# Optimization experiments

Measured on AMD Instinct MI355X. Metric: run time of the kernel, lower is better.

## Reference

```python
import jax, jax.numpy as jnp
import numpy as np

S = 4096
V = 50000
E = 512
H = 512
CE = 128
CH = 128
T = 50


def _lstm_dir(x, W_ih, W_hh, b, reverse):
    # x: [S, D]; PyTorch gate order i, f, g, o. b = b_ih + b_hh fused.
    gx = x @ W_ih.T + b  # [S, 4H] precomputed input contribution
    Hd = W_hh.shape[1]
    def step(carry, g_t):
        h, c = carry
        g = g_t + h @ W_hh.T
        i, f, gg, o = jnp.split(g, 4, axis=-1)
        c = jax.nn.sigmoid(f) * c + jax.nn.sigmoid(i) * jnp.tanh(gg)
        h = jax.nn.sigmoid(o) * jnp.tanh(c)
        return (h, c), h
    init = (jnp.zeros((Hd,), x.dtype), jnp.zeros((Hd,), x.dtype))
    _, hs = jax.lax.scan(step, init, gx, reverse=reverse)
    return hs  # [S, H]


def _bilstm(x, Wih_f, Whh_f, b_f, Wih_b, Whh_b, b_b):
    fwd = _lstm_dir(x, Wih_f, Whh_f, b_f, False)
    bwd = _lstm_dir(x, Wih_b, Whh_b, b_b, True)
    return jnp.concatenate([fwd, bwd], axis=-1)  # [S, 2H]


def _viterbi(emissions, start_t, end_t, trans):
    # emissions: [S, T]. Standard CRF Viterbi (torchcrf semantics).
    score0 = start_t + emissions[0]  # [T]
    def step(score, emit):
        m = score[:, None] + trans          # [T_prev, T_cur]
        bp = jnp.argmax(m, axis=0)          # best previous tag for each cur tag
        new_score = jnp.max(m, axis=0) + emit
        return new_score, bp
    final, bps = jax.lax.scan(step, score0, emissions[1:])  # bps: [S-1, T]
    final = final + end_t
    last = jnp.argmax(final)
    def back(tag, bp):
        prev = bp[tag]
        return prev, prev
    _, path_head = jax.lax.scan(back, last, bps, reverse=True)  # [S-1]
    return jnp.concatenate([path_head, last[None]])  # [S]


def setup_inputs() -> dict:
    key = jax.random.key(0)
    ks = jax.random.split(key, 20)
    s = 0.05
    inp = {
        'sentence': jax.random.randint(ks[0], (S,), 0, V),
        'char_sentence': jax.random.randint(ks[1], (S,), 0, V),
        'word_emb': jax.random.normal(ks[2], (V, E), jnp.float32) * s,
        'char_emb': jax.random.normal(ks[3], (V, CE), jnp.float32) * s,
        # char BiLSTM
        'cWih_f': jax.random.normal(ks[4], (4 * CH, CE), jnp.float32) * s,
        'cWhh_f': jax.random.normal(ks[5], (4 * CH, CH), jnp.float32) * s,
        'cb_f': jnp.zeros((4 * CH,), jnp.float32),
        'cWih_b': jax.random.normal(ks[6], (4 * CH, CE), jnp.float32) * s,
        'cWhh_b': jax.random.normal(ks[7], (4 * CH, CH), jnp.float32) * s,
        'cb_b': jnp.zeros((4 * CH,), jnp.float32),
        # word BiLSTM (input dim E + 2*CH)
        'wWih_f': jax.random.normal(ks[8], (4 * H, E + 2 * CH), jnp.float32) * s,
        'wWhh_f': jax.random.normal(ks[9], (4 * H, H), jnp.float32) * s,
        'wb_f': jnp.zeros((4 * H,), jnp.float32),
        'wWih_b': jax.random.normal(ks[10], (4 * H, E + 2 * CH), jnp.float32) * s,
        'wWhh_b': jax.random.normal(ks[11], (4 * H, H), jnp.float32) * s,
        'wb_b': jnp.zeros((4 * H,), jnp.float32),
        # hidden2tag
        'W_tag': jax.random.normal(ks[12], (T, 2 * H), jnp.float32) * s,
        'b_tag': jnp.zeros((T,), jnp.float32),
        # CRF params
        'start_t': jax.random.normal(ks[13], (T,), jnp.float32) * s,
        'end_t': jax.random.normal(ks[14], (T,), jnp.float32) * s,
        'trans': jax.random.normal(ks[15], (T, T), jnp.float32) * s,
    }
    return inp


def reference(sentence, char_sentence, word_emb, char_emb,
              cWih_f, cWhh_f, cb_f, cWih_b, cWhh_b, cb_b,
              wWih_f, wWhh_f, wb_f, wWih_b, wWhh_b, wb_b,
              W_tag, b_tag, start_t, end_t, trans):
    we = word_emb[sentence]          # [S, E]
    ce = char_emb[char_sentence]     # [S, CE]
    char_out = _bilstm(ce, cWih_f, cWhh_f, cb_f, cWih_b, cWhh_b, cb_b)  # [S, 2*CH]
    emb = jnp.concatenate([we, char_out], axis=-1)  # [S, E + 2*CH]
    lstm_out = _bilstm(emb, wWih_f, wWhh_f, wb_f, wWih_b, wWhh_b, wb_b)  # [S, 2H]
    tag_space = lstm_out @ W_tag.T + b_tag  # [S, T] emissions
    path = _viterbi(tag_space, start_t, end_t, trans)  # [S] int32 tags
    return path
```

## Files before the change

kernel.cpp:

```cpp
#include <hip/hip_runtime.h>
#include <math.h>

#define SQ   4096
#define EDIM 512
#define CEDIM 128
#define CHH  128
#define WH   512
#define NT   50

typedef unsigned long long ull;

__device__ __forceinline__ float sigf(float x) { return 1.0f / (1.0f + expf(-x)); }

#define PIN4(V) asm volatile("" : "+v"(V.x), "+v"(V.y), "+v"(V.z), "+v"(V.w));

__device__ __forceinline__ void ld8x_sc0(const ull* p, ull& q0, ull& q1, ull& q2,
                                         ull& q3, ull& q4, ull& q5, ull& q6, ull& q7) {
    asm volatile("global_load_dwordx2 %0, %8, off sc0\n\t"
                 "global_load_dwordx2 %1, %8, off offset:8 sc0\n\t"
                 "global_load_dwordx2 %2, %8, off offset:16 sc0\n\t"
                 "global_load_dwordx2 %3, %8, off offset:24 sc0\n\t"
                 "global_load_dwordx2 %4, %8, off offset:32 sc0\n\t"
                 "global_load_dwordx2 %5, %8, off offset:40 sc0\n\t"
                 "global_load_dwordx2 %6, %8, off offset:48 sc0\n\t"
                 "global_load_dwordx2 %7, %8, off offset:56 sc0\n\t"
                 "s_waitcnt vmcnt(0)"
                 : "=&v"(q0), "=&v"(q1), "=&v"(q2), "=&v"(q3),
                   "=&v"(q4), "=&v"(q5), "=&v"(q6), "=&v"(q7)
                 : "v"(p) : "memory");
}
__device__ __forceinline__ ull ld_mir(const ull* p) {
    return __hip_atomic_load(p, __ATOMIC_RELAXED, __HIP_MEMORY_SCOPE_AGENT);
}
__device__ __forceinline__ void st_plain8(ull* p, ull v) {
    asm volatile("global_store_dwordx2 %0, %1, off" :: "v"(p), "v"(v) : "memory");
}
__device__ __forceinline__ void st_mir(ull* p, ull v) {
    __hip_atomic_store(p, v, __ATOMIC_RELAXED, __HIP_MEMORY_SCOPE_AGENT);
}
__device__ __forceinline__ unsigned umin2(unsigned a, unsigned b) { return a < b ? a : b; }

#define FMA4(W, off) { float4 h4 = *(const float4*)&hc[off]; \
    a0 += W.x * h4.x; a1 += W.y * h4.y; a2 += W.z * h4.z; a3 += W.w * h4.w; }

__global__ __launch_bounds__(256) void k1_gather_cgx(
    const int* __restrict__ sent, const int* __restrict__ csent,
    const float* __restrict__ wemb, const float* __restrict__ cemb,
    const float* __restrict__ cWih_f, const float* __restrict__ cb_f,
    const float* __restrict__ cWih_b, const float* __restrict__ cb_b,
    float* __restrict__ we_g, float* __restrict__ cgx)
{
    const int tid = threadIdx.x;
    const int t0 = blockIdx.x * 16;
    __shared__ __align__(16) float ceL[16][128];
    __shared__ int sids[16], cids[16];
    if (tid < 16) sids[tid] = sent[t0 + tid];
    else if (tid < 32) cids[tid - 16] = csent[t0 + tid - 16];
    __syncthreads();
    {
        int f4 = tid;
        for (int q = 0; q < 2; ++q, f4 += 256) {
            int r = f4 >> 5, k4 = f4 & 31;
            float4 v = *(const float4*)&cemb[(size_t)cids[r] * CEDIM + k4 * 4];
            *(float4*)&ceL[r][k4 * 4] = v;
        }
    }
    {
        int f4 = tid;
        for (int q = 0; q < 8; ++q, f4 += 256) {
            int r = f4 >> 7, k4 = f4 & 127;
            float4 v = *(const float4*)&wemb[(size_t)sids[r] * EDIM + k4 * 4];
            *(float4*)&we_g[(size_t)(t0 + r) * EDIM + k4 * 4] = v;
        }
    }
    __syncthreads();
    for (int q = 0; q < 4; ++q) {
        int j = q * 256 + tid;
        int d = j >> 9, r = j & 511;
        const float* Wih = d ? cWih_b : cWih_f;
        const float* cb = d ? cb_b : cb_f;
        float b = cb[r];
        float acc[16];
#pragma unroll
        for (int tt = 0; tt < 16; ++tt) acc[tt] = b;
        for (int k4 = 0; k4 < 32; ++k4) {
            float4 wv = *(const float4*)&Wih[r * CEDIM + k4 * 4];
#pragma unroll
            for (int tt = 0; tt < 16; ++tt) {
                acc[tt] += wv.x * ceL[tt][k4 * 4 + 0] + wv.y * ceL[tt][k4 * 4 + 1]
                         + wv.z * ceL[tt][k4 * 4 + 2] + wv.w * ceL[tt][k4 * 4 + 3];
            }
        }
#pragma unroll
        for (int tt = 0; tt < 16; ++tt)
            cgx[((size_t)d * SQ + (t0 + tt)) * 512 + r] = acc[tt];
    }
}

__global__ __launch_bounds__(1024, 4) void k2_charlstm_gemm(
    const float* __restrict__ cWhh_f, const float* __restrict__ cWhh_b,
    const float* __restrict__ cgx, float* __restrict__ cho,
    const float* __restrict__ we_g,
    const float* __restrict__ wWih_f, const float* __restrict__ wb_f,
    const float* __restrict__ wWih_b, const float* __restrict__ wb_b,
    float* __restrict__ wgx)
{
    const int tid = threadIdx.x;
    __shared__ __align__(16) float At[32][68];
    __shared__ __align__(16) float Bt[32][128];
    __shared__ __align__(16) float hstC[128];
    __shared__ float partC[2][516];
    __shared__ float trC[512];

    if (blockIdx.x < 2) {
        const int dir = blockIdx.x;
        const float* Whh = dir ? cWhh_b : cWhh_f;
        const int row = tid & 511;
        const int half = tid >> 9;
        const float4* wp = (const float4*)&Whh[(size_t)row * CHH + half * 64];
        float4 w0 = wp[0], w1 = wp[1], w2 = wp[2], w3 = wp[3];
        float4 w4 = wp[4], w5 = wp[5], w6 = wp[6], w7 = wp[7];
        float4 w8 = wp[8], w9 = wp[9], w10 = wp[10], w11 = wp[11];
        float4 w12 = wp[12], w13 = wp[13], w14 = wp[14], w15 = wp[15];
        PIN4(w0) PIN4(w1) PIN4(w2) PIN4(w3) PIN4(w4) PIN4(w5) PIN4(w6) PIN4(w7)
        PIN4(w8) PIN4(w9) PIN4(w10) PIN4(w11) PIN4(w12) PIN4(w13) PIN4(w14) PIN4(w15)

        const float* gxc = cgx + (size_t)dir * SQ * 512;
        float cst = 0.f;
        if (tid < 32) *(float4*)&hstC[tid * 4] = make_float4(0, 0, 0, 0);
        __syncthreads();
        for (int t = 0; t < SQ; ++t) {
            const int x = dir ? (SQ - 1 - t) : t;
            float gxv = (tid < 512) ? gxc[(size_t)x * 512 + tid] : 0.f;
            float a0 = 0.f, a1 = 0.f, a2 = 0.f, a3 = 0.f;
            const float* hc = &hstC[half * 64];
            FMA4(w0, 0)   FMA4(w1, 4)   FMA4(w2, 8)   FMA4(w3, 12)
            FMA4(w4, 16)  FMA4(w5, 20)  FMA4(w6, 24)  FMA4(w7, 28)
            FMA4(w8, 32)  FMA4(w9, 36)  FMA4(w10, 40) FMA4(w11, 44)
            FMA4(w12, 48) FMA4(w13, 52) FMA4(w14, 56) FMA4(w15, 60)
            partC[half][row] = (a0 + a1) + (a2 + a3);
            __syncthreads();
            if (tid < 512) {
                float s = partC[0][tid] + partC[1][tid] + gxv;
                const bool isg = ((tid >> 7) == 2);
                float y = sigf(isg ? (s + s) : s);
                trC[tid] = isg ? (y + y - 1.f) : y;
            }
            __syncthreads();
            if (tid < 128) {
                float iv = trC[tid], fv = trC[128 + tid];
                float gv = trC[256 + tid], ov = trC[384 + tid];
                cst = fv * cst + iv * gv;
                float ts = sigf(cst + cst);
                float h = ov * (ts + ts - 1.f);
                hstC[tid] = h;
                cho[(size_t)x * 256 + dir * CHH + tid] = h;
            }
            __syncthreads();
        }
        return;
    }
    const int tile = blockIdx.x - 2;
    const int dir = tile >> 10;
    const int rem = tile & 1023;
    const int mb = rem >> 4;
    const int nb = rem & 15;
    const float* Wih = dir ? wWih_b : wWih_f;
    const float* wb = dir ? wb_b : wb_f;
    float* C = wgx + (size_t)dir * SQ * 2048;
    const int tm = tid >> 6, tn = tid & 63;
    float acc[4][2];
#pragma unroll
    for (int i = 0; i < 4; ++i) { acc[i][0] = 0.f; acc[i][1] = 0.f; }
    for (int kb = 0; kb < 16; ++kb) {
        if (tid < 512) {
            int rowm = tid >> 3, k4 = tid & 7;
            float4 v = *(const float4*)&we_g[(size_t)(mb * 64 + rowm) * EDIM + kb * 32 + k4 * 4];
            At[k4 * 4 + 0][rowm] = v.x; At[k4 * 4 + 1][rowm] = v.y;
            At[k4 * 4 + 2][rowm] = v.z; At[k4 * 4 + 3][rowm] = v.w;
        }
        {
            int rr = tid >> 3, k4 = tid & 7;
            float4 v = *(const float4*)&Wih[(size_t)(nb * 128 + rr) * 768 + kb * 32 + k4 * 4];
            Bt[k4 * 4 + 0][rr] = v.x; Bt[k4 * 4 + 1][rr] = v.y;
            Bt[k4 * 4 + 2][rr] = v.z; Bt[k4 * 4 + 3][rr] = v.w;
        }
        __syncthreads();
#pragma unroll
        for (int kk = 0; kk < 32; ++kk) {
            float4 a4 = *(const float4*)&At[kk][tm * 4];
            float2 b2 = *(const float2*)&Bt[kk][tn * 2];
            acc[0][0] += a4.x * b2.x; acc[0][1] += a4.x * b2.y;
            acc[1][0] += a4.y * b2.x; acc[1][1] += a4.y * b2.y;
            acc[2][0] += a4.z * b2.x; acc[2][1] += a4.z * b2.y;
            acc[3][0] += a4.w * b2.x; acc[3][1] += a4.w * b2.y;
        }
        __syncthreads();
    }
    float2 wbv = *(const float2*)&wb[nb * 128 + tn * 2];
#pragma unroll
    for (int i = 0; i < 4; ++i) {
        float2 o;
        o.x = acc[i][0] + wbv.x; o.y = acc[i][1] + wbv.y;
        *(float2*)&C[(size_t)(mb * 64 + tm * 4 + i) * 2048 + nb * 128 + tn * 2] = o;
    }
}

__global__ __launch_bounds__(512, 2) void k3_gemm_char(
    const float* __restrict__ cho,
    const float* __restrict__ wWih_f, const float* __restrict__ wWih_b,
    float* __restrict__ wgx)
{
    const int tid = threadIdx.x;
    const int tile = blockIdx.x;
    const int dir = tile >> 10;
    const int rem = tile & 1023;
    const int mb = rem >> 4, nb = rem & 15;
    const float* Wih = dir ? wWih_b : wWih_f;
    float* C = wgx + (size_t)dir * SQ * 2048;
    __shared__ __align__(16) float At[32][68];
    __shared__ __align__(16) float Bt[32][128];
    const int tm = tid >> 5, tn = tid & 31;
    float acc[4][4];
#pragma unroll
    for (int i = 0; i < 4; ++i)
#pragma unroll
        for (int jj = 0; jj < 4; ++jj) acc[i][jj] = 0.f;
    for (int kb = 0; kb < 8; ++kb) {
        {
            int rowm = tid >> 3, k4 = tid & 7;
            float4 v = *(const float4*)&cho[(size_t)(mb * 64 + rowm) * 256 + kb * 32 + k4 * 4];
            At[k4 * 4 + 0][rowm] = v.x; At[k4 * 4 + 1][rowm] = v.y;
            At[k4 * 4 + 2][rowm] = v.z; At[k4 * 4 + 3][rowm] = v.w;
        }
#pragma unroll
        for (int q = 0; q < 2; ++q) {
            int f4 = q * 512 + tid;
            int rr = f4 >> 3, k4 = f4 & 7;
            float4 v = *(const float4*)&Wih[(size_t)(nb * 128 + rr) * 768 + 512 + kb * 32 + k4 * 4];
            Bt[k4 * 4 + 0][rr] = v.x; Bt[k4 * 4 + 1][rr] = v.y;
            Bt[k4 * 4 + 2][rr] = v.z; Bt[k4 * 4 + 3][rr] = v.w;
        }
        __syncthreads();
#pragma unroll
        for (int kk = 0; kk < 32; ++kk) {
            float4 a4 = *(const float4*)&At[kk][tm * 4];
            float4 b4 = *(const float4*)&Bt[kk][tn * 4];
            acc[0][0] += a4.x * b4.x; acc[0][1] += a4.x * b4.y; acc[0][2] += a4.x * b4.z; acc[0][3] += a4.x * b4.w;
            acc[1][0] += a4.y * b4.x; acc[1][1] += a4.y * b4.y; acc[1][2] += a4.y * b4.z; acc[1][3] += a4.y * b4.w;
            acc[2][0] += a4.z * b4.x; acc[2][1] += a4.z * b4.y; acc[2][2] += a4.z * b4.z; acc[2][3] += a4.z * b4.w;
            acc[3][0] += a4.w * b4.x; acc[3][1] += a4.w * b4.y; acc[3][2] += a4.w * b4.z; acc[3][3] += a4.w * b4.w;
        }
        __syncthreads();
    }
#pragma unroll
    for (int i = 0; i < 4; ++i) {
        float* cp = &C[(size_t)(mb * 64 + tm * 4 + i) * 2048 + nb * 128 + tn * 4];
        float4 o = *(float4*)cp;
        o.x += acc[i][0]; o.y += acc[i][1]; o.z += acc[i][2]; o.w += acc[i][3];
        *(float4*)cp = o;
    }
}

__global__ __launch_bounds__(1024, 4) void k4_word_lstm(
    const float* __restrict__ wWhh_f, const float* __restrict__ wWhh_b,
    const float* __restrict__ wgx, float* __restrict__ lstm, ull* __restrict__ pairs)
{
    const int res = blockIdx.x & 7;
    if (res > 1) return;
    const int dir = res;
    const int wid = blockIdx.x >> 3;
    const int tid = threadIdx.x;
    const int k = tid >> 6;
    const int r = tid & 63;
    const int g = r >> 4, u = r & 15;
    const float* Whh = dir ? wWhh_b : wWhh_f;
    const int G = g * WH + wid * 16 + u;
    const float4* wp = (const float4*)&Whh[(size_t)G * WH + k * 32];
    float4 w0 = wp[0], w1 = wp[1], w2 = wp[2], w3 = wp[3];
    float4 w4 = wp[4], w5 = wp[5], w6 = wp[6], w7 = wp[7];
    PIN4(w0) PIN4(w1) PIN4(w2) PIN4(w3) PIN4(w4) PIN4(w5) PIN4(w6) PIN4(w7)

    __shared__ __align__(16) float hst[512];
    __shared__ float part[16][65];

    ull* wpf = pairs;
    ull* wpm = pairs + 2048;
    const float* gx = wgx + (size_t)dir * SQ * 2048;
    float cst = 0.f;
    int useFast = 1, alive = 1;
    for (int t = 0; t < SQ; ++t) {
        const int x = dir ? (SQ - 1 - t) : t;
        float gxv = 0.f;
        if (tid < 64)
            gxv = gx[(size_t)x * 2048 + (size_t)(tid >> 4) * 512 + wid * 16 + (tid & 15)];
        if (t == 0) {
            if (tid < 128) *(float4*)&hst[tid * 4] = make_float4(0, 0, 0, 0);
        } else if (tid < 64) {
            const size_t boff = ((size_t)((t - 1) & 1) * 2 + dir) * 512 + tid * 8;
            const ull* pf = wpf + boff;
            const ull* pm = wpm + boff;
            ull q0 = 0, q1 = 0, q2 = 0, q3 = 0, q4 = 0, q5 = 0, q6 = 0, q7 = 0;
            int spins = 0;
            while (alive) {
                if (useFast) {
                    ld8x_sc0(pf, q0, q1, q2, q3, q4, q5, q6, q7);
                } else {
                    q0 = ld_mir(pm + 0); q1 = ld_mir(pm + 1);
                    q2 = ld_mir(pm + 2); q3 = ld_mir(pm + 3);
                    q4 = ld_mir(pm + 4); q5 = ld_mir(pm + 5);
                    q6 = ld_mir(pm + 6); q7 = ld_mir(pm + 7);
                }
                unsigned tm = umin2(umin2(umin2((unsigned)(q0 >> 32), (unsigned)(q1 >> 32)),
                                          umin2((unsigned)(q2 >> 32), (unsigned)(q3 >> 32))),
                                    umin2(umin2((unsigned)(q4 >> 32), (unsigned)(q5 >> 32)),
                                          umin2((unsigned)(q6 >> 32), (unsigned)(q7 >> 32))));
                if (__all(tm >= (unsigned)t)) break;
                ++spins;
                if (useFast && spins > 2048) { useFast = 0; spins = 0; }
                if (!useFast && spins > (1 << 20)) alive = 0;
                __builtin_amdgcn_s_sleep(1);
            }
            float* hd = &hst[tid * 8];
            hd[0] = __uint_as_float((unsigned)q0); hd[1] = __uint_as_float((unsigned)q1);
            hd[2] = __uint_as_float((unsigned)q2); hd[3] = __uint_as_float((unsigned)q3);
            hd[4] = __uint_as_float((unsigned)q4); hd[5] = __uint_as_float((unsigned)q5);
            hd[6] = __uint_as_float((unsigned)q6); hd[7] = __uint_as_float((unsigned)q7);
        }
        __syncthreads();
        float a0 = 0.f, a1 = 0.f, a2 = 0.f, a3 = 0.f;
        const float* hc = &hst[k * 32];
        FMA4(w0, 0)  FMA4(w1, 4)  FMA4(w2, 8)  FMA4(w3, 12)
        FMA4(w4, 16) FMA4(w5, 20) FMA4(w6, 24) FMA4(w7, 28)
        part[k][r] = (a0 + a1) + (a2 + a3);
        __syncthreads();
        if (tid < 64) {
            float s = gxv;
#pragma unroll
            for (int kk = 0; kk < 16; ++kk) s += part[kk][tid];
            const bool isg = ((tid >> 4) == 2);
            float y = sigf(isg ? (s + s) : s);
            float val = isg ? (y + y - 1.f) : y;
            float fv = __shfl(val, 16 + (tid & 15));
            float gv = __shfl(val, 32 + (tid & 15));
            float ov = __shfl(val, 48 + (tid & 15));
            if (tid < 16) {
                cst = fv * cst + val * gv;
                float ts = sigf(cst + cst);
                float h = ov * (ts + ts - 1.f);
                const int unit = wid * 16 + tid;
                lstm[(size_t)x * 1024 + dir * WH + unit] = h;
                ull q = ((ull)(unsigned)(t + 1) << 32) | (ull)__float_as_uint(h);
                const size_t poff = ((size_t)(t & 1) * 2 + dir) * 512 + unit;
                st_plain8(wpf + poff, q);
                st_mir(wpm + poff, q);
            }
        }
    }
}

__global__ __launch_bounds__(64) void k5_emis(
    const float* __restrict__ lstm, const float* __restrict__ Wtag,
    const float* __restrict__ btag, float* __restrict__ emis)
{
    const int t = blockIdx.x, tid = threadIdx.x;
    __shared__ __align__(16) float rowL[1024];
#pragma unroll
    for (int q = 0; q < 4; ++q) {
        int f4 = q * 64 + tid;
        *(float4*)&rowL[f4 * 4] = *(const float4*)&lstm[(size_t)t * 1024 + f4 * 4];
    }
    __syncthreads();
    if (tid < NT) {
        float a0 = 0.f, a1 = 0.f, a2 = 0.f, a3 = 0.f;
        const float* wr = Wtag + (size_t)tid * 1024;
        for (int k4 = 0; k4 < 256; ++k4) {
            float4 wv = *(const float4*)&wr[k4 * 4];
            a0 += wv.x * rowL[k4 * 4 + 0];
            a1 += wv.y * rowL[k4 * 4 + 1];
            a2 += wv.z * rowL[k4 * 4 + 2];
            a3 += wv.w * rowL[k4 * 4 + 3];
        }
        emis[(size_t)t * NT + tid] = btag[tid] + (a0 + a1) + (a2 + a3);
    }
}

__global__ __launch_bounds__(256) void k6a_viterbi(
    const float* __restrict__ emis, const float* __restrict__ start_t,
    const float* __restrict__ end_t, const float* __restrict__ trans,
    unsigned char* __restrict__ bpb, int* __restrict__ last)
{
    const int tid = threadIdx.x;
    const int g = tid >> 6, c = tid & 63;
    __shared__ float sc[64];
    __shared__ float pbest[4][64];
    __shared__ int pbp[4][64];
    const int p0 = g * 13;
    float tr[13];
#pragma unroll
    for (int i = 0; i < 13; ++i) {
        int p = p0 + i;
        tr[i] = (c < NT && p < NT) ? trans[p * NT + c] : -1e30f;
    }
    if (tid < 64) sc[tid] = (tid < NT) ? (start_t[tid] + emis[tid]) : -1e30f;
    __syncthreads();
    for (int t = 1; t < SQ; ++t) {
        float best = -1e30f; int bp = 0;
#pragma unroll
        for (int i = 0; i < 13; ++i) {
            float v = sc[p0 + i] + tr[i];
            if (v > best) { best = v; bp = p0 + i; }
        }
        pbest[g][c] = best; pbp[g][c] = bp;
        __syncthreads();
        if (tid < NT) {
            float b = pbest[0][tid]; int bb = pbp[0][tid];
#pragma unroll
            for (int gg = 1; gg < 4; ++gg) {
                float v = pbest[gg][tid];
                if (v > b) { b = v; bb = pbp[gg][tid]; }
            }
            bpb[(size_t)t * NT + tid] = (unsigned char)bb;
            sc[tid] = b + emis[(size_t)t * NT + tid];
        }
        __syncthreads();
    }
    if (tid == 0) {
        float b = -1e30f; int bi = 0;
        for (int cc = 0; cc < NT; ++cc) {
            float v = sc[cc] + end_t[cc];
            if (v > b) { b = v; bi = cc; }
        }
        *last = bi;
    }
}

__global__ __launch_bounds__(64) void k6b_maps(
    const unsigned char* __restrict__ bpb, int* __restrict__ map_)
{
    const int k = blockIdx.x;
    const int e = threadIdx.x;
    if (k == 0 || e >= NT) return;
    int tag = e;
    for (int i = 63; i >= 0; --i) {
        int t = k * 64 + i;
        tag = bpb[(size_t)t * NT + tag];
    }
    map_[k * NT + e] = tag;
}

__global__ __launch_bounds__(64) void k6c_backtrack(
    const unsigned char* __restrict__ bpb, const int* __restrict__ map_,
    const int* __restrict__ last, int* __restrict__ path)
{
    __shared__ int B[64];
    if (threadIdx.x == 0) {
        int tag = *last;
        B[63] = tag;
        for (int k = 63; k >= 1; --k) {
            tag = map_[k * NT + tag];
            B[k - 1] = tag;
        }
    }
    __syncthreads();
    const int k = threadIdx.x;
    int tag = B[k];
    for (int i = 63; i >= 0; --i) {
        int t = k * 64 + i;
        path[t] = tag;
        if (t >= 1) tag = bpb[(size_t)t * NT + tag];
    }
}

extern "C" void kernel_launch(void* const* d_in, const int* in_sizes, int n_in,
                              void* d_out, int out_size, void* d_ws, size_t ws_size,
                              hipStream_t stream)
{
    const int* sent = (const int*)d_in[0];
    const int* csent = (const int*)d_in[1];
    const float* wemb = (const float*)d_in[2];
    const float* cemb = (const float*)d_in[3];
    const float* cWih_f = (const float*)d_in[4];
    const float* cWhh_f = (const float*)d_in[5];
    const float* cb_f = (const float*)d_in[6];
    const float* cWih_b = (const float*)d_in[7];
    const float* cWhh_b = (const float*)d_in[8];
    const float* cb_b = (const float*)d_in[9];
    const float* wWih_f = (const float*)d_in[10];
    const float* wWhh_f = (const float*)d_in[11];
    const float* wb_f = (const float*)d_in[12];
    const float* wWih_b = (const float*)d_in[13];
    const float* wWhh_b = (const float*)d_in[14];
    const float* wb_b = (const float*)d_in[15];
    const float* Wtag = (const float*)d_in[16];
    const float* btag = (const float*)d_in[17];
    const float* start_t = (const float*)d_in[18];
    const float* end_t = (const float*)d_in[19];
    const float* trans = (const float*)d_in[20];
    int* path = (int*)d_out;

    float* ws = (float*)d_ws;
    float* we_g = ws;
    float* cgx  = we_g + (size_t)SQ * EDIM;
    float* cho  = cgx + (size_t)2 * SQ * 512;
    float* wgx  = cho + (size_t)SQ * 256;
    float* lstm = wgx + (size_t)2 * SQ * 2048;
    float* emis = lstm + (size_t)SQ * 1024;
    ull* pairs  = (ull*)(emis + (size_t)SQ * NT);
    int* map_   = (int*)(pairs + 5120);
    int* lastp  = map_ + 64 * NT;
    unsigned char* bpb = (unsigned char*)(lastp + 4);

    (void)hipMemsetAsync(pairs, 0, 5120 * sizeof(ull), stream);

    k1_gather_cgx<<<SQ / 16, 256, 0, stream>>>(sent, csent, wemb, cemb,
                                               cWih_f, cb_f, cWih_b, cb_b, we_g, cgx);
    k2_charlstm_gemm<<<2 + 2048, 1024, 0, stream>>>(cWhh_f, cWhh_b, cgx, cho, we_g,
                                                    wWih_f, wb_f, wWih_b, wb_b, wgx);
    k3_gemm_char<<<2048, 512, 0, stream>>>(cho, wWih_f, wWih_b, wgx);
    k4_word_lstm<<<256, 1024, 0, stream>>>(wWhh_f, wWhh_b, wgx, lstm, pairs);
    k5_emis<<<SQ, 64, 0, stream>>>(lstm, Wtag, btag, emis);
    k6a_viterbi<<<1, 256, 0, stream>>>(emis, start_t, end_t, trans, bpb, lastp);
    k6b_maps<<<64, 64, 0, stream>>>(bpb, map_);
    k6c_backtrack<<<1, 64, 0, stream>>>(bpb, map_, lastp, path);
}
```

Measured before the change: 14.14 ms.

## Let each wave poll its own h slice and drop a barrier in LSTM loops

```diff
diff --git a/kernel.cpp b/kernel.cpp
--- a/kernel.cpp
+++ b/kernel.cpp
@@ -14,20 +14,9 @@
 
 #define PIN4(V) asm volatile("" : "+v"(V.x), "+v"(V.y), "+v"(V.z), "+v"(V.w));
 
-__device__ __forceinline__ void ld8x_sc0(const ull* p, ull& q0, ull& q1, ull& q2,
-                                         ull& q3, ull& q4, ull& q5, ull& q6, ull& q7) {
-    asm volatile("global_load_dwordx2 %0, %8, off sc0\n\t"
-                 "global_load_dwordx2 %1, %8, off offset:8 sc0\n\t"
-                 "global_load_dwordx2 %2, %8, off offset:16 sc0\n\t"
-                 "global_load_dwordx2 %3, %8, off offset:24 sc0\n\t"
-                 "global_load_dwordx2 %4, %8, off offset:32 sc0\n\t"
-                 "global_load_dwordx2 %5, %8, off offset:40 sc0\n\t"
-                 "global_load_dwordx2 %6, %8, off offset:48 sc0\n\t"
-                 "global_load_dwordx2 %7, %8, off offset:56 sc0\n\t"
-                 "s_waitcnt vmcnt(0)"
-                 : "=&v"(q0), "=&v"(q1), "=&v"(q2), "=&v"(q3),
-                   "=&v"(q4), "=&v"(q5), "=&v"(q6), "=&v"(q7)
-                 : "v"(p) : "memory");
+__device__ __forceinline__ ull ld1_sc0(const ull* p) {
+    ull q; asm volatile("global_load_dwordx2 %0, %1, off sc0\n\ts_waitcnt vmcnt(0)"
+                        : "=v"(q) : "v"(p) : "memory"); return q;
 }
 __device__ __forceinline__ ull ld_mir(const ull* p) {
     return __hip_atomic_load(p, __ATOMIC_RELAXED, __HIP_MEMORY_SCOPE_AGENT);
@@ -38,7 +27,6 @@
 __device__ __forceinline__ void st_mir(ull* p, ull v) {
     __hip_atomic_store(p, v, __ATOMIC_RELAXED, __HIP_MEMORY_SCOPE_AGENT);
 }
-__device__ __forceinline__ unsigned umin2(unsigned a, unsigned b) { return a < b ? a : b; }
 
 #define FMA4(W, off) { float4 h4 = *(const float4*)&hc[off]; \
     a0 += W.x * h4.x; a1 += W.y * h4.y; a2 += W.z * h4.z; a3 += W.w * h4.w; }
@@ -110,7 +98,6 @@
     __shared__ __align__(16) float Bt[32][128];
     __shared__ __align__(16) float hstC[128];
     __shared__ float partC[2][516];
-    __shared__ float trC[512];
 
     if (blockIdx.x < 2) {
         const int dir = blockIdx.x;
@@ -127,29 +114,38 @@
 
         const float* gxc = cgx + (size_t)dir * SQ * 512;
         float cst = 0.f;
+        float gxp0 = 0.f, gxp1 = 0.f;
+        if (tid < 512) {
+            gxp0 = gxc[(size_t)(dir ? (SQ - 1) : 0) * 512 + tid];
+            gxp1 = gxc[(size_t)(dir ? (SQ - 2) : 1) * 512 + tid];
+        }
         if (tid < 32) *(float4*)&hstC[tid * 4] = make_float4(0, 0, 0, 0);
         __syncthreads();
         for (int t = 0; t < SQ; ++t) {
             const int x = dir ? (SQ - 1 - t) : t;
-            float gxv = (tid < 512) ? gxc[(size_t)x * 512 + tid] : 0.f;
+            float gxv = gxp0;
+            gxp0 = gxp1;
+            if (tid < 512 && t + 2 < SQ) {
+                const int x2 = dir ? (SQ - 3 - t) : (t + 2);
+                gxp1 = gxc[(size_t)x2 * 512 + tid];
+            }
             float a0 = 0.f, a1 = 0.f, a2 = 0.f, a3 = 0.f;
             const float* hc = &hstC[half * 64];
             FMA4(w0, 0)   FMA4(w1, 4)   FMA4(w2, 8)   FMA4(w3, 12)
             FMA4(w4, 16)  FMA4(w5, 20)  FMA4(w6, 24)  FMA4(w7, 28)
             FMA4(w8, 32)  FMA4(w9, 36)  FMA4(w10, 40) FMA4(w11, 44)
             FMA4(w12, 48) FMA4(w13, 52) FMA4(w14, 56) FMA4(w15, 60)
-            partC[half][row] = (a0 + a1) + (a2 + a3);
-            __syncthreads();
-            if (tid < 512) {
-                float s = partC[0][tid] + partC[1][tid] + gxv;
-                const bool isg = ((tid >> 7) == 2);
-                float y = sigf(isg ? (s + s) : s);
-                trC[tid] = isg ? (y + y - 1.f) : y;
-            }
+            float dot = (a0 + a1) + (a2 + a3);
+            partC[half][row] = half ? dot : (dot + gxv);
             __syncthreads();
             if (tid < 128) {
-                float iv = trC[tid], fv = trC[128 + tid];
-                float gv = trC[256 + tid], ov = trC[384 + tid];
+                float siv = partC[0][tid]       + partC[1][tid];
+                float sfv = partC[0][128 + tid] + partC[1][128 + tid];
+                float sgv = partC[0][256 + tid] + partC[1][256 + tid];
+                float sov = partC[0][384 + tid] + partC[1][384 + tid];
+                float iv = sigf(siv), fv = sigf(sfv), ov = sigf(sov);
+                float yg = sigf(sgv + sgv);
+                float gv = yg + yg - 1.f;
                 cst = fv * cst + iv * gv;
                 float ts = sigf(cst + cst);
                 float h = ov * (ts + ts - 1.f);
@@ -272,8 +268,8 @@
     const int wid = blockIdx.x >> 3;
     const int tid = threadIdx.x;
     const int k = tid >> 6;
-    const int r = tid & 63;
-    const int g = r >> 4, u = r & 15;
+    const int lane = tid & 63;
+    const int g = lane >> 4, u = lane & 15;
     const float* Whh = dir ? wWhh_b : wWhh_f;
     const int G = g * WH + wid * 16 + u;
     const float4* wp = (const float4*)&Whh[(size_t)G * WH + k * 32];
@@ -282,7 +278,7 @@
     PIN4(w0) PIN4(w1) PIN4(w2) PIN4(w3) PIN4(w4) PIN4(w5) PIN4(w6) PIN4(w7)
 
     __shared__ __align__(16) float hst[512];
-    __shared__ float part[16][65];
+    __shared__ float part[2][16][65];
 
     ull* wpf = pairs;
     ull* wpm = pairs + 2048;
@@ -293,67 +289,52 @@
         const int x = dir ? (SQ - 1 - t) : t;
         float gxv = 0.f;
         if (tid < 64)
-            gxv = gx[(size_t)x * 2048 + (size_t)(tid >> 4) * 512 + wid * 16 + (tid & 15)];
+            gxv = gx[(size_t)x * 2048 + (size_t)g * 512 + wid * 16 + u];
         if (t == 0) {
-            if (tid < 128) *(float4*)&hst[tid * 4] = make_float4(0, 0, 0, 0);
-        } else if (tid < 64) {
-            const size_t boff = ((size_t)((t - 1) & 1) * 2 + dir) * 512 + tid * 8;
+            if (lane < 32) hst[k * 32 + lane] = 0.f;
+        } else {
+            const size_t boff = ((size_t)((t - 1) & 1) * 2 + dir) * 512 + k * 32 + (lane & 31);
             const ull* pf = wpf + boff;
             const ull* pm = wpm + boff;
-            ull q0 = 0, q1 = 0, q2 = 0, q3 = 0, q4 = 0, q5 = 0, q6 = 0, q7 = 0;
+            ull q = 0;
             int spins = 0;
             while (alive) {
-                if (useFast) {
-                    ld8x_sc0(pf, q0, q1, q2, q3, q4, q5, q6, q7);
-                } else {
-                    q0 = ld_mir(pm + 0); q1 = ld_mir(pm + 1);
-                    q2 = ld_mir(pm + 2); q3 = ld_mir(pm + 3);
-                    q4 = ld_mir(pm + 4); q5 = ld_mir(pm + 5);
-                    q6 = ld_mir(pm + 6); q7 = ld_mir(pm + 7);
-                }
-                unsigned tm = umin2(umin2(umin2((unsigned)(q0 >> 32), (unsigned)(q1 >> 32)),
-                                          umin2((unsigned)(q2 >> 32), (unsigned)(q3 >> 32))),
-                                    umin2(umin2((unsigned)(q4 >> 32), (unsigned)(q5 >> 32)),
-                                          umin2((unsigned)(q6 >> 32), (unsigned)(q7 >> 32))));
-                if (__all(tm >= (unsigned)t)) break;
+                q = useFast ? ld1_sc0(pf) : ld_mir(pm);
+                if (__all((unsigned)(q >> 32) >= (unsigned)t)) break;
                 ++spins;
-                if (useFast && spins > 2048) { useFast = 0; spins = 0; }
+                if (useFast && spins > 4096) { useFast = 0; spins = 0; }
                 if (!useFast && spins > (1 << 20)) alive = 0;
                 __builtin_amdgcn_s_sleep(1);
             }
-            float* hd = &hst[tid * 8];
-            hd[0] = __uint_as_float((unsigned)q0); hd[1] = __uint_as_float((unsigned)q1);
-            hd[2] = __uint_as_float((unsigned)q2); hd[3] = __uint_as_float((unsigned)q3);
-            hd[4] = __uint_as_float((unsigned)q4); hd[5] = __uint_as_float((unsigned)q5);
-            hd[6] = __uint_as_float((unsigned)q6); hd[7] = __uint_as_float((unsigned)q7);
-        }
-        __syncthreads();
+            if (lane < 32) hst[k * 32 + lane] = __uint_as_float((unsigned)q);
+        }
         float a0 = 0.f, a1 = 0.f, a2 = 0.f, a3 = 0.f;
         const float* hc = &hst[k * 32];
         FMA4(w0, 0)  FMA4(w1, 4)  FMA4(w2, 8)  FMA4(w3, 12)
         FMA4(w4, 16) FMA4(w5, 20) FMA4(w6, 24) FMA4(w7, 28)
-        part[k][r] = (a0 + a1) + (a2 + a3);
+        part[t & 1][k][lane] = (a0 + a1) + (a2 + a3);
         __syncthreads();
         if (tid < 64) {
             float s = gxv;
-#pragma unroll
-            for (int kk = 0; kk < 16; ++kk) s += part[kk][tid];
-            const bool isg = ((tid >> 4) == 2);
+            const float (*pp)[65] = part[t & 1];
+#pragma unroll
+            for (int kk = 0; kk < 16; ++kk) s += pp[kk][tid];
+            const bool isg = (g == 2);
             float y = sigf(isg ? (s + s) : s);
             float val = isg ? (y + y - 1.f) : y;
-            float fv = __shfl(val, 16 + (tid & 15));
-            float gv = __shfl(val, 32 + (tid & 15));
-            float ov = __shfl(val, 48 + (tid & 15));
+            float fv = __shfl(val, 16 + u);
+            float gv = __shfl(val, 32 + u);
+            float ov = __shfl(val, 48 + u);
             if (tid < 16) {
                 cst = fv * cst + val * gv;
                 float ts = sigf(cst + cst);
                 float h = ov * (ts + ts - 1.f);
                 const int unit = wid * 16 + tid;
                 lstm[(size_t)x * 1024 + dir * WH + unit] = h;
-                ull q = ((ull)(unsigned)(t + 1) << 32) | (ull)__float_as_uint(h);
+                ull qq = ((ull)(unsigned)(t + 1) << 32) | (ull)__float_as_uint(h);
                 const size_t poff = ((size_t)(t & 1) * 2 + dir) * 512 + unit;
-                st_plain8(wpf + poff, q);
-                st_mir(wpm + poff, q);
+                st_plain8(wpf + poff, qq);
+                st_mir(wpm + poff, qq);
             }
         }
     }
```

Result: slower. 15.27 ms (+8.0%).
